# Performance work log

Measured on AMD Instinct MI355X. Metric: run time of the kernel, lower is better.

The kernel has to match this reference:

```python
import jax, jax.numpy as jnp
import numpy as np

TOP_K = 2  # config.num_experts_per_tok


def setup_inputs() -> dict:
    key = jax.random.key(0)
    ks = jax.random.split(key, 5)
    B, S, H, F, E = 1, 2048, 2048, 1408, 8
    sc_h = 1.0 / np.sqrt(H)
    sc_f = 1.0 / np.sqrt(F)
    return {
        "hidden_states": jax.random.normal(ks[0], (B, S, H), jnp.float32),
        "gate_w": jax.random.normal(ks[1], (E, H), jnp.float32) * sc_h,
        "w1": jax.random.normal(ks[2], (E, F, H), jnp.float32) * sc_h,
        "w3": jax.random.normal(ks[3], (E, F, H), jnp.float32) * sc_h,
        "w2": jax.random.normal(ks[4], (E, H, F), jnp.float32) * sc_f,
    }


def reference(hidden_states, gate_w, w1, w3, w2):
    B, S, H = hidden_states.shape
    x = hidden_states.reshape(-1, H)            # [T, H]
    T = x.shape[0]
    E = gate_w.shape[0]

    # Router: logits -> fp32 softmax -> top-k -> renormalize
    router_logits = x @ gate_w.T                # [T, E]
    probs = jax.nn.softmax(router_logits.astype(jnp.float32), axis=-1)
    topk_w, topk_idx = jax.lax.top_k(probs, TOP_K)          # [T, K]
    topk_w = topk_w / topk_w.sum(axis=-1, keepdims=True)
    topk_w = topk_w.astype(x.dtype)

    # Scatter top-k weights into a dense [T, E] combine matrix (zero elsewhere)
    w_full = jnp.zeros((T, E), x.dtype).at[jnp.arange(T)[:, None], topk_idx].add(topk_w)

    # Per-expert SwiGLU MLP applied to all tokens; masked combine honors routing.
    g = jnp.einsum('th,efh->etf', x, w1)        # [E, T, F]
    u = jnp.einsum('th,efh->etf', x, w3)        # [E, T, F]
    h = jax.nn.silu(g) * u                      # [E, T, F]
    y = jnp.einsum('etf,ehf->eth', h, w2)       # [E, T, H]
    out = jnp.einsum('eth,te->th', y, w_full)   # [T, H]

    final_hidden_states = out.reshape(B, S, H)
    return final_hidden_states, router_logits
```

## Files before the change

kernel.cpp:

```cpp
#include <hip/hip_runtime.h>
#include <hip/hip_bf16.h>

#define T_TOK 2048
#define H_DIM 2048
#define F_DIM 1408
#define N_EXP 8
#define BM 128
#define BN 64
#define BK 64

#define NITEM 40
#define G1_NY (F_DIM / BN)
#define G2_NY (H_DIM / BN)
#define G1_CHUNK ((NITEM * G1_NY) / 8)
#define G2_CHUNK ((NITEM * G2_NY) / 8)
#define WELEMS ((size_t)N_EXP * F_DIM * H_DIM)

typedef float f32x4 __attribute__((ext_vector_type(4)));
typedef short s16x8 __attribute__((ext_vector_type(8)));
typedef unsigned int u32;

#define LOFF(row, kbyte) (((row) << 7) + ((kbyte) ^ (((row) & 7) << 4)))

__device__ __forceinline__ int bf2i(__hip_bfloat162 h) {
  int r; __builtin_memcpy(&r, &h, 4); return r;
}

__device__ __forceinline__ int4 pack8(float4 a, float4 b) {
  int4 r;
  r.x = bf2i(__float22bfloat162_rn(float2{a.x, a.y}));
  r.y = bf2i(__float22bfloat162_rn(float2{a.z, a.w}));
  r.z = bf2i(__float22bfloat162_rn(float2{b.x, b.y}));
  r.w = bf2i(__float22bfloat162_rn(float2{b.z, b.w}));
  return r;
}

__device__ __forceinline__ unsigned short f2bf(float f) {
  __hip_bfloat16 h = __float2bfloat16(f);
  unsigned short r; __builtin_memcpy(&r, &h, 2); return r;
}

__device__ __forceinline__ f32x4 mfma16(s16x8 a, s16x8 b, f32x4 c) {
  return __builtin_amdgcn_mfma_f32_16x16x32_bf16(a, b, c, 0, 0, 0);
}

__device__ __forceinline__ void dma16(const unsigned short* g, unsigned short* l) {
  __builtin_amdgcn_global_load_lds((const __attribute__((address_space(1))) u32*)g,
                                   (__attribute__((address_space(3))) u32*)l, 16, 0, 0);
}

__global__ void cast_w3(const float* __restrict__ wa, const float* __restrict__ wb,
                        const float* __restrict__ wc,
                        unsigned short* __restrict__ oa, unsigned short* __restrict__ ob,
                        unsigned short* __restrict__ oc, int n8) {
  const float* in = (blockIdx.y == 0) ? wa : (blockIdx.y == 1) ? wb : wc;
  unsigned short* out = (blockIdx.y == 0) ? oa : (blockIdx.y == 1) ? ob : oc;
  int i = blockIdx.x * blockDim.x + threadIdx.x;
  const int stride = gridDim.x * blockDim.x;
  for (; i < n8; i += stride) {
    const float4 a = ((const float4*)in)[2 * i];
    const float4 b = ((const float4*)in)[2 * i + 1];
    ((int4*)out)[i] = pack8(a, b);
  }
}

__global__ void router_kernel(const float* __restrict__ x, const float* __restrict__ gw,
                              float* __restrict__ logits, int* __restrict__ tk_idx,
                              float* __restrict__ tk_w, unsigned short* __restrict__ xb) {
  __shared__ float xs[H_DIM];
  __shared__ float lg[N_EXP];
  const int t = blockIdx.x;
  const int tid = threadIdx.x;
  const float4 xv = ((const float4*)(x + (size_t)t * H_DIM))[tid];
  ((float4*)xs)[tid] = xv;
  int2 cw;
  cw.x = bf2i(__float22bfloat162_rn(float2{xv.x, xv.y}));
  cw.y = bf2i(__float22bfloat162_rn(float2{xv.z, xv.w}));
  ((int2*)(xb + (size_t)t * H_DIM))[tid] = cw;
  __syncthreads();
  const int w = tid >> 6, l = tid & 63;
  const float* g = gw + w * H_DIM;
  float s = 0.f;
  for (int j = l; j < H_DIM; j += 64) s += xs[j] * g[j];
#pragma unroll
  for (int o = 32; o; o >>= 1) s += __shfl_down(s, o);
  if (l == 0) lg[w] = s;
  __syncthreads();
  if (tid == 0) {
    float mx = lg[0];
#pragma unroll
    for (int i = 1; i < N_EXP; i++) mx = fmaxf(mx, lg[i]);
    float p[N_EXP];
#pragma unroll
    for (int i = 0; i < N_EXP; i++) p[i] = __expf(lg[i] - mx);
    int i0 = 0;
#pragma unroll
    for (int i = 1; i < N_EXP; i++) if (p[i] > p[i0]) i0 = i;
    int i1 = (i0 == 0) ? 1 : 0;
#pragma unroll
    for (int i = 0; i < N_EXP; i++) if (i != i0 && p[i] > p[i1]) i1 = i;
    const float ww = p[i0] + p[i1];
    tk_idx[t * 2] = i0; tk_idx[t * 2 + 1] = i1;
    tk_w[t * 2] = p[i0] / ww; tk_w[t * 2 + 1] = p[i1] / ww;
#pragma unroll
    for (int i = 0; i < N_EXP; i++) logits[t * N_EXP + i] = lg[i];
  }
}

__global__ void build_lists(const int* __restrict__ tk_idx, const float* __restrict__ tk_w,
                            int* __restrict__ counts, int* __restrict__ entries,
                            float* __restrict__ wlist) {
  const int e = blockIdx.x;
  const int l = threadIdx.x;
  int base = 0;
  for (int t0 = 0; t0 < T_TOK; t0 += 64) {
    const int t = t0 + l;
    int sel = -1; float w = 0.f;
    const int i0 = tk_idx[t * 2], i1 = tk_idx[t * 2 + 1];
    if (i0 == e) { sel = t * 2; w = tk_w[t * 2]; }
    else if (i1 == e) { sel = t * 2 + 1; w = tk_w[t * 2 + 1]; }
    const unsigned long long mask = __ballot(sel >= 0);
    const int pos = base + __popcll(mask & ((1ull << l) - 1ull));
    if (sel >= 0) { entries[e * T_TOK + pos] = sel; wlist[e * T_TOK + pos] = w; }
    base += __popcll(mask);
  }
  if (l == 0) counts[e] = base;
}

__global__ void build_items(const int* __restrict__ counts, int* __restrict__ items) {
  if (threadIdx.x == 0) {
    int n = 0;
#pragma unroll
    for (int e = 0; e < N_EXP; e++) {
      const int c = counts[e];
      for (int m0 = 0; m0 < c; m0 += BM) items[1 + n++] = (e << 16) | (m0 / BM);
    }
    items[0] = n;
  }
}

__global__ __launch_bounds__(512)
void moe_gemm1b(const unsigned short* __restrict__ w1b, const unsigned short* __restrict__ w3b,
                const unsigned short* __restrict__ xb,
                const int* __restrict__ counts, const int* __restrict__ entries,
                const int* __restrict__ items,
                unsigned short* __restrict__ hb) {
  const int lin = blockIdx.x;
  const int virt = (lin & 7) * G1_CHUNK + (lin >> 3);
  const int ix = virt % NITEM;
  const int iy = virt / NITEM;
  if (ix >= items[0]) return;
  const int it = items[1 + ix];
  const int e = it >> 16;
  const int m0 = (it & 0xffff) * BM;
  const int rem = counts[e] - m0;
  const int n0 = iy * BN;

  __shared__ unsigned short sA[2][BM * BK];
  __shared__ unsigned short sB1[3][BN * BK];
  __shared__ unsigned short sB3[3][BN * BK];

  const int tid = threadIdx.x;
  const int lane = tid & 63;
  const int wave = tid >> 6;
  const int wm = wave >> 1, wn = wave & 1;

  const int* elist = entries + e * T_TOK + m0;

  const int gcolb = (((lane & 7) << 4) ^ (((lane >> 3) & 7) << 4));
  const int arow0 = wave * 16 + (lane >> 3);
  const int arow1 = arow0 + 8;
  const int tokA0 = elist[arow0 < rem ? arow0 : 0] >> 1;
  const int tokA1 = elist[arow1 < rem ? arow1 : 0] >> 1;
  const unsigned short* gaA0 = xb + (size_t)tokA0 * H_DIM + (gcolb >> 1);
  const unsigned short* gaA1 = xb + (size_t)tokA1 * H_DIM + (gcolb >> 1);
  const int awA = wave * 1024;

  const int rB = tid >> 3;
  const int gbcol = ((tid & 7) ^ (rB & 7)) * 8;
  const unsigned short* gb1 = w1b + ((size_t)e * F_DIM + n0 + rB) * H_DIM + gbcol;
  const unsigned short* gb3 = w3b + ((size_t)e * F_DIM + n0 + rB) * H_DIM + gbcol;
  const int awB = wave * 512;

  const int rowA0 = wm * 32 + (lane & 15);
  const int rowA1 = rowA0 + 16;
  const int rowB0 = wn * 32 + (lane & 15);
  const int rowB1 = rowB0 + 16;
  const int kb = (lane >> 4) * 16;

  const f32x4 zero = {0.f, 0.f, 0.f, 0.f};
  f32x4 aG[2][2], aU[2][2];
#pragma unroll
  for (int i = 0; i < 2; i++)
#pragma unroll
    for (int j = 0; j < 2; j++) { aG[i][j] = zero; aU[i][j] = zero; }

  dma16(gaA0, sA[0] + awA);
  dma16(gaA1, sA[0] + awA + 512);
  dma16(gb1, sB1[0] + awB);
  dma16(gb3, sB3[0] + awB);
  asm volatile("s_waitcnt vmcnt(0)" ::: "memory");
  __builtin_amdgcn_s_barrier();
  dma16(gb1 + BK, sB1[1] + awB);
  dma16(gb3 + BK, sB3[1] + awB);

  const int NT = H_DIM / BK;
  int bi = 0;
  for (int t = 0; t < NT; ++t) {
    const int an = (t + 1) & 1;
    const int bw = (bi + 2 >= 3) ? (bi - 1) : (bi + 2);
    const int ka = (t + 1 < NT) ? (t + 1) * BK : 0;
    const int kbv = (t + 2 < NT) ? (t + 2) * BK : 0;
    dma16(gaA0 + ka, sA[an] + awA);
    dma16(gaA1 + ka, sA[an] + awA + 512);
    dma16(gb1 + kbv, sB1[bw] + awB);
    dma16(gb3 + kbv, sB3[bw] + awB);
    __builtin_amdgcn_sched_barrier(0);
    __builtin_amdgcn_s_setprio(1);
    const char* aC = (const char*)sA[t & 1];
    const char* b1C = (const char*)sB1[bi];
    const char* b3C = (const char*)sB3[bi];
#pragma unroll
    for (int kk = 0; kk < 2; kk++) {
      const int kbyte = kk * 64 + kb;
      const s16x8 a0 = *(const s16x8*)(aC + LOFF(rowA0, kbyte));
      const s16x8 a1 = *(const s16x8*)(aC + LOFF(rowA1, kbyte));
      const s16x8 p0 = *(const s16x8*)(b1C + LOFF(rowB0, kbyte));
      const s16x8 p1 = *(const s16x8*)(b1C + LOFF(rowB1, kbyte));
      const s16x8 q0 = *(const s16x8*)(b3C + LOFF(rowB0, kbyte));
      const s16x8 q1 = *(const s16x8*)(b3C + LOFF(rowB1, kbyte));
      aG[0][0] = mfma16(a0, p0, aG[0][0]); aG[0][1] = mfma16(a0, p1, aG[0][1]);
      aG[1][0] = mfma16(a1, p0, aG[1][0]); aG[1][1] = mfma16(a1, p1, aG[1][1]);
      aU[0][0] = mfma16(a0, q0, aU[0][0]); aU[0][1] = mfma16(a0, q1, aU[0][1]);
      aU[1][0] = mfma16(a1, q0, aU[1][0]); aU[1][1] = mfma16(a1, q1, aU[1][1]);
    }
    __builtin_amdgcn_s_setprio(0);
    asm volatile("s_waitcnt vmcnt(2) lgkmcnt(0)" ::: "memory");
    __builtin_amdgcn_s_barrier();
    bi = (bi + 1 >= 3) ? 0 : (bi + 1);
  }

#pragma unroll
  for (int i = 0; i < 2; i++) {
#pragma unroll
    for (int r = 0; r < 4; r++) {
      const int m = wm * 32 + i * 16 + ((lane >> 4) << 2) + r;
      if (m < rem) {
        const int entry = elist[m];
        unsigned short* hp = hb + (size_t)entry * F_DIM + n0 + wn * 32 + (lane & 15);
#pragma unroll
        for (int j = 0; j < 2; j++) {
          const float g = aG[i][j][r];
          const float u = aU[i][j][r];
          hp[j * 16] = f2bf(g / (1.f + __expf(-g)) * u);
        }
      }
    }
  }
}

__global__ __launch_bounds__(512)
void moe_gemm2b(const unsigned short* __restrict__ w2b,
                const unsigned short* __restrict__ hb,
                const int* __restrict__ counts, const int* __restrict__ entries,
                const float* __restrict__ wlist, const int* __restrict__ items,
                float* __restrict__ out) {
  const int lin = blockIdx.x;
  const int virt = (lin & 7) * G2_CHUNK + (lin >> 3);
  const int ix = virt % NITEM;
  const int iy = virt / NITEM;
  if (ix >= items[0]) return;
  const int it = items[1 + ix];
  const int e = it >> 16;
  const int m0 = (it & 0xffff) * BM;
  const int rem = counts[e] - m0;
  const int n0 = iy * BN;

  __shared__ unsigned short sA[2][BM * BK];
  __shared__ unsigned short sB[3][BN * BK];

  const int tid = threadIdx.x;
  const int lane = tid & 63;
  const int wave = tid >> 6;
  const int wm = wave >> 1, wn = wave & 1;

  const int* elist = entries + e * T_TOK + m0;
  const float* wl = wlist + e * T_TOK + m0;

  const int gcolb = (((lane & 7) << 4) ^ (((lane >> 3) & 7) << 4));
  const int arow0 = wave * 16 + (lane >> 3);
  const int arow1 = arow0 + 8;
  const int enA0 = elist[arow0 < rem ? arow0 : 0];
  const int enA1 = elist[arow1 < rem ? arow1 : 0];
  const unsigned short* gaA0 = hb + (size_t)enA0 * F_DIM + (gcolb >> 1);
  const unsigned short* gaA1 = hb + (size_t)enA1 * F_DIM + (gcolb >> 1);
  const int awA = wave * 1024;

  const int rB = tid >> 3;
  const int gbcol = ((tid & 7) ^ (rB & 7)) * 8;
  const unsigned short* gb = w2b + ((size_t)e * H_DIM + n0 + rB) * F_DIM + gbcol;
  const int awB = wave * 512;

  const int rowA0 = wm * 32 + (lane & 15);
  const int rowA1 = rowA0 + 16;
  const int rowB0 = wn * 32 + (lane & 15);
  const int rowB1 = rowB0 + 16;
  const int kb = (lane >> 4) * 16;

  const f32x4 zero = {0.f, 0.f, 0.f, 0.f};
  f32x4 ac[2][2];
#pragma unroll
  for (int i = 0; i < 2; i++)
#pragma unroll
    for (int j = 0; j < 2; j++) ac[i][j] = zero;

  dma16(gaA0, sA[0] + awA);
  dma16(gaA1, sA[0] + awA + 512);
  dma16(gb, sB[0] + awB);
  asm volatile("s_waitcnt vmcnt(0)" ::: "memory");
  __builtin_amdgcn_s_barrier();
  dma16(gb + BK, sB[1] + awB);

  const int NT = F_DIM / BK;
  int bi = 0;
  for (int t = 0; t < NT; ++t) {
    const int an = (t + 1) & 1;
    const int bw = (bi + 2 >= 3) ? (bi - 1) : (bi + 2);
    const int ka = (t + 1 < NT) ? (t + 1) * BK : 0;
    const int kbv = (t + 2 < NT) ? (t + 2) * BK : 0;
    dma16(gaA0 + ka, sA[an] + awA);
    dma16(gaA1 + ka, sA[an] + awA + 512);
    dma16(gb + kbv, sB[bw] + awB);
    __builtin_amdgcn_sched_barrier(0);
    __builtin_amdgcn_s_setprio(1);
    const char* aC = (const char*)sA[t & 1];
    const char* bC = (const char*)sB[bi];
#pragma unroll
    for (int kk = 0; kk < 2; kk++) {
      const int kbyte = kk * 64 + kb;
      const s16x8 a0 = *(const s16x8*)(aC + LOFF(rowA0, kbyte));
      const s16x8 a1 = *(const s16x8*)(aC + LOFF(rowA1, kbyte));
      const s16x8 f0 = *(const s16x8*)(bC + LOFF(rowB0, kbyte));
      const s16x8 f1 = *(const s16x8*)(bC + LOFF(rowB1, kbyte));
      ac[0][0] = mfma16(a0, f0, ac[0][0]); ac[0][1] = mfma16(a0, f1, ac[0][1]);
      ac[1][0] = mfma16(a1, f0, ac[1][0]); ac[1][1] = mfma16(a1, f1, ac[1][1]);
    }
    __builtin_amdgcn_s_setprio(0);
    asm volatile("s_waitcnt vmcnt(1) lgkmcnt(0)" ::: "memory");
    __builtin_amdgcn_s_barrier();
    bi = (bi + 1 >= 3) ? 0 : (bi + 1);
  }

#pragma unroll
  for (int i = 0; i < 2; i++) {
#pragma unroll
    for (int r = 0; r < 4; r++) {
      const int m = wm * 32 + i * 16 + ((lane >> 4) << 2) + r;
      if (m < rem) {
        const int entry = elist[m];
        const int tok = entry >> 1;
        const float wgt = wl[m];
        float* op = out + (size_t)tok * H_DIM + n0 + wn * 32 + (lane & 15);
#pragma unroll
        for (int j = 0; j < 2; j++) atomicAdd(op + j * 16, wgt * ac[i][j][r]);
      }
    }
  }
}

extern "C" void kernel_launch(void* const* d_in, const int* in_sizes, int n_in,
                              void* d_out, int out_size, void* d_ws, size_t ws_size,
                              hipStream_t stream) {
  const float* x  = (const float*)d_in[0];
  const float* gw = (const float*)d_in[1];
  const float* w1 = (const float*)d_in[2];
  const float* w3 = (const float*)d_in[3];
  const float* w2 = (const float*)d_in[4];
  float* out = (float*)d_out;
  float* logits = out + (size_t)T_TOK * H_DIM;

  char* ws = (char*)d_ws;
  size_t off = 0;
  unsigned short* xb = (unsigned short*)(ws + off); off += (size_t)T_TOK * H_DIM * 2;
  unsigned short* hb = (unsigned short*)(ws + off); off += (size_t)T_TOK * 2 * F_DIM * 2;
  int*   tk_idx = (int*)(ws + off);   off += (size_t)T_TOK * 2 * 4;
  float* tk_w   = (float*)(ws + off); off += (size_t)T_TOK * 2 * 4;
  int*   counts = (int*)(ws + off);   off += 256;
  int*   entries = (int*)(ws + off);  off += (size_t)N_EXP * T_TOK * 4;
  float* wlist  = (float*)(ws + off); off += (size_t)N_EXP * T_TOK * 4;
  int*   items  = (int*)(ws + off);   off += 256;
  unsigned short* w1b = (unsigned short*)(ws + off); off += WELEMS * 2;
  unsigned short* w3b = (unsigned short*)(ws + off); off += WELEMS * 2;
  unsigned short* w2b = (unsigned short*)(ws + off); off += WELEMS * 2;

  (void)hipMemsetAsync(d_out, 0, (size_t)out_size * sizeof(float), stream);
  const int n8 = (int)(WELEMS / 8);
  cast_w3<<<dim3(2048, 3), 256, 0, stream>>>(w1, w3, w2, w1b, w3b, w2b, n8);
  router_kernel<<<dim3(T_TOK), 512, 0, stream>>>(x, gw, logits, tk_idx, tk_w, xb);
  build_lists<<<dim3(N_EXP), 64, 0, stream>>>(tk_idx, tk_w, counts, entries, wlist);
  build_items<<<dim3(1), 64, 0, stream>>>(counts, items);
  moe_gemm1b<<<dim3(NITEM * G1_NY), 512, 0, stream>>>(w1b, w3b, xb, counts, entries, items, hb);
  moe_gemm2b<<<dim3(NITEM * G2_NY), 512, 0, stream>>>(w2b, hb, counts, entries, wlist, items, out);
}
```

Baseline: 285.2 us.

## Fuse w2 fp32-to-bf16 conversion into second GEMM and double-buffer first GEMM

The separate cast pass over w2 is removed. The second expert GEMM now loads fp32 w2 tiles into registers, packs them to bf16 and stores them into LDS, with a register prefetch pipeline spanning two steps. This avoids writing and re-reading a bf16 copy of w2. The first GEMM drops from a triple-buffered to a double-buffered B pipeline that waits on all loads each step, which cuts LDS use but may expose more load latency. The fused path reads w2 in fp32, so each tile fetched by the GEMM carries twice the bytes, and w2 tiles are reread across token blocks.

```diff
diff --git a/kernel.cpp b/kernel.cpp
--- a/kernel.cpp
+++ b/kernel.cpp
@@ -49,12 +49,11 @@
                                    (__attribute__((address_space(3))) u32*)l, 16, 0, 0);
 }
 
-__global__ void cast_w3(const float* __restrict__ wa, const float* __restrict__ wb,
-                        const float* __restrict__ wc,
-                        unsigned short* __restrict__ oa, unsigned short* __restrict__ ob,
-                        unsigned short* __restrict__ oc, int n8) {
-  const float* in = (blockIdx.y == 0) ? wa : (blockIdx.y == 1) ? wb : wc;
-  unsigned short* out = (blockIdx.y == 0) ? oa : (blockIdx.y == 1) ? ob : oc;
+__global__ void cast_w2buf(const float* __restrict__ wa, const float* __restrict__ wb,
+                           unsigned short* __restrict__ oa, unsigned short* __restrict__ ob,
+                           int n8) {
+  const float* in = (blockIdx.y == 0) ? wa : wb;
+  unsigned short* out = (blockIdx.y == 0) ? oa : ob;
   int i = blockIdx.x * blockDim.x + threadIdx.x;
   const int stride = gridDim.x * blockDim.x;
   for (; i < n8; i += stride) {
@@ -157,8 +156,8 @@
   const int n0 = iy * BN;
 
   __shared__ unsigned short sA[2][BM * BK];
-  __shared__ unsigned short sB1[3][BN * BK];
-  __shared__ unsigned short sB3[3][BN * BK];
+  __shared__ unsigned short sB1[2][BN * BK];
+  __shared__ unsigned short sB3[2][BN * BK];
 
   const int tid = threadIdx.x;
   const int lane = tid & 63;
@@ -201,25 +200,20 @@
   dma16(gb3, sB3[0] + awB);
   asm volatile("s_waitcnt vmcnt(0)" ::: "memory");
   __builtin_amdgcn_s_barrier();
-  dma16(gb1 + BK, sB1[1] + awB);
-  dma16(gb3 + BK, sB3[1] + awB);
 
   const int NT = H_DIM / BK;
-  int bi = 0;
   for (int t = 0; t < NT; ++t) {
-    const int an = (t + 1) & 1;
-    const int bw = (bi + 2 >= 3) ? (bi - 1) : (bi + 2);
-    const int ka = (t + 1 < NT) ? (t + 1) * BK : 0;
-    const int kbv = (t + 2 < NT) ? (t + 2) * BK : 0;
-    dma16(gaA0 + ka, sA[an] + awA);
-    dma16(gaA1 + ka, sA[an] + awA + 512);
-    dma16(gb1 + kbv, sB1[bw] + awB);
-    dma16(gb3 + kbv, sB3[bw] + awB);
+    const int cur = t & 1, nxt = cur ^ 1;
+    const int kn = (t + 1 < NT) ? (t + 1) * BK : 0;
+    dma16(gaA0 + kn, sA[nxt] + awA);
+    dma16(gaA1 + kn, sA[nxt] + awA + 512);
+    dma16(gb1 + kn, sB1[nxt] + awB);
+    dma16(gb3 + kn, sB3[nxt] + awB);
     __builtin_amdgcn_sched_barrier(0);
     __builtin_amdgcn_s_setprio(1);
-    const char* aC = (const char*)sA[t & 1];
-    const char* b1C = (const char*)sB1[bi];
-    const char* b3C = (const char*)sB3[bi];
+    const char* aC = (const char*)sA[cur];
+    const char* b1C = (const char*)sB1[cur];
+    const char* b3C = (const char*)sB3[cur];
 #pragma unroll
     for (int kk = 0; kk < 2; kk++) {
       const int kbyte = kk * 64 + kb;
@@ -235,9 +229,8 @@
       aU[1][0] = mfma16(a1, q0, aU[1][0]); aU[1][1] = mfma16(a1, q1, aU[1][1]);
     }
     __builtin_amdgcn_s_setprio(0);
-    asm volatile("s_waitcnt vmcnt(2) lgkmcnt(0)" ::: "memory");
+    asm volatile("s_waitcnt vmcnt(0) lgkmcnt(0)" ::: "memory");
     __builtin_amdgcn_s_barrier();
-    bi = (bi + 1 >= 3) ? 0 : (bi + 1);
   }
 
 #pragma unroll
@@ -259,8 +252,36 @@
   }
 }
 
+#define G2F_STEP(ARD, AWR, BLR, BLW, RS, KA1_, KB3_)                          \
+  {                                                                           \
+    asm volatile("s_waitcnt vmcnt(2) lgkmcnt(0)" ::: "memory");               \
+    __builtin_amdgcn_s_barrier();                                             \
+    *(int4*)((BLW) + offB) = pack8(RS[0], RS[1]);                             \
+    {                                                                         \
+      const int ka = (KA1_);                                                  \
+      dma16(ga0 + ka, (AWR) + aw);                                            \
+      dma16(ga1 + ka, (AWR) + aw + 512);                                      \
+      const int kbl = (KB3_);                                                 \
+      RS[0] = *(const float4*)(pb + kbl);                                     \
+      RS[1] = *(const float4*)(pb + kbl + 4);                                 \
+    }                                                                         \
+    __builtin_amdgcn_sched_barrier(0);                                        \
+    __builtin_amdgcn_s_setprio(1);                                            \
+    _Pragma("unroll")                                                         \
+    for (int kk = 0; kk < 2; kk++) {                                          \
+      const int kbyte = kk * 64 + kb;                                         \
+      const s16x8 a0 = *(const s16x8*)((const char*)(ARD) + LOFF(rowA0, kbyte)); \
+      const s16x8 a1 = *(const s16x8*)((const char*)(ARD) + LOFF(rowA1, kbyte)); \
+      const s16x8 f0 = *(const s16x8*)((BLR) + LOFF(rowB0, kbyte));           \
+      const s16x8 f1 = *(const s16x8*)((BLR) + LOFF(rowB1, kbyte));           \
+      ac[0][0] = mfma16(a0, f0, ac[0][0]); ac[0][1] = mfma16(a0, f1, ac[0][1]); \
+      ac[1][0] = mfma16(a1, f0, ac[1][0]); ac[1][1] = mfma16(a1, f1, ac[1][1]); \
+    }                                                                         \
+    __builtin_amdgcn_s_setprio(0);                                            \
+  }
+
 __global__ __launch_bounds__(512)
-void moe_gemm2b(const unsigned short* __restrict__ w2b,
+void moe_gemm2f(const float* __restrict__ w2,
                 const unsigned short* __restrict__ hb,
                 const int* __restrict__ counts, const int* __restrict__ entries,
                 const float* __restrict__ wlist, const int* __restrict__ items,
@@ -277,7 +298,8 @@
   const int n0 = iy * BN;
 
   __shared__ unsigned short sA[2][BM * BK];
-  __shared__ unsigned short sB[3][BN * BK];
+  __shared__ unsigned short sB[2][BN * BK];
+  char* sb0 = (char*)sB[0]; char* sb1 = (char*)sB[1];
 
   const int tid = threadIdx.x;
   const int lane = tid & 63;
@@ -287,19 +309,19 @@
   const int* elist = entries + e * T_TOK + m0;
   const float* wl = wlist + e * T_TOK + m0;
 
-  const int gcolb = (((lane & 7) << 4) ^ (((lane >> 3) & 7) << 4));
+  const int r0 = tid >> 3;
+  const int gc = tid & 7;
+  const float* pb = w2 + ((size_t)e * H_DIM + n0 + r0) * F_DIM + gc * 8;
+  const int offB = LOFF(r0, gc * 16);
+
   const int arow0 = wave * 16 + (lane >> 3);
   const int arow1 = arow0 + 8;
+  const int gcolb = (((lane & 7) << 4) ^ (((lane >> 3) & 7) << 4));
   const int enA0 = elist[arow0 < rem ? arow0 : 0];
   const int enA1 = elist[arow1 < rem ? arow1 : 0];
-  const unsigned short* gaA0 = hb + (size_t)enA0 * F_DIM + (gcolb >> 1);
-  const unsigned short* gaA1 = hb + (size_t)enA1 * F_DIM + (gcolb >> 1);
-  const int awA = wave * 1024;
-
-  const int rB = tid >> 3;
-  const int gbcol = ((tid & 7) ^ (rB & 7)) * 8;
-  const unsigned short* gb = w2b + ((size_t)e * H_DIM + n0 + rB) * F_DIM + gbcol;
-  const int awB = wave * 512;
+  const unsigned short* ga0 = hb + (size_t)enA0 * F_DIM + (gcolb >> 1);
+  const unsigned short* ga1 = hb + (size_t)enA1 * F_DIM + (gcolb >> 1);
+  const int aw = wave * 1024;
 
   const int rowA0 = wm * 32 + (lane & 15);
   const int rowA1 = rowA0 + 16;
@@ -314,41 +336,23 @@
 #pragma unroll
     for (int j = 0; j < 2; j++) ac[i][j] = zero;
 
-  dma16(gaA0, sA[0] + awA);
-  dma16(gaA1, sA[0] + awA + 512);
-  dma16(gb, sB[0] + awB);
-  asm volatile("s_waitcnt vmcnt(0)" ::: "memory");
-  __builtin_amdgcn_s_barrier();
-  dma16(gb + BK, sB[1] + awB);
+  float4 s1r[2], s0r[2];
+  s1r[0] = *(const float4*)(pb);      s1r[1] = *(const float4*)(pb + 4);
+  s0r[0] = *(const float4*)(pb + BK); s0r[1] = *(const float4*)(pb + BK + 4);
+  dma16(ga0, sA[0] + aw);
+  dma16(ga1, sA[0] + aw + 512);
+  asm volatile("s_waitcnt vmcnt(4)" ::: "memory");
+  *(int4*)(sb0 + offB) = pack8(s1r[0], s1r[1]);
+  s1r[0] = *(const float4*)(pb + 2 * BK); s1r[1] = *(const float4*)(pb + 2 * BK + 4);
 
   const int NT = F_DIM / BK;
-  int bi = 0;
-  for (int t = 0; t < NT; ++t) {
-    const int an = (t + 1) & 1;
-    const int bw = (bi + 2 >= 3) ? (bi - 1) : (bi + 2);
-    const int ka = (t + 1 < NT) ? (t + 1) * BK : 0;
-    const int kbv = (t + 2 < NT) ? (t + 2) * BK : 0;
-    dma16(gaA0 + ka, sA[an] + awA);
-    dma16(gaA1 + ka, sA[an] + awA + 512);
-    dma16(gb + kbv, sB[bw] + awB);
-    __builtin_amdgcn_sched_barrier(0);
-    __builtin_amdgcn_s_setprio(1);
-    const char* aC = (const char*)sA[t & 1];
-    const char* bC = (const char*)sB[bi];
-#pragma unroll
-    for (int kk = 0; kk < 2; kk++) {
-      const int kbyte = kk * 64 + kb;
-      const s16x8 a0 = *(const s16x8*)(aC + LOFF(rowA0, kbyte));
-      const s16x8 a1 = *(const s16x8*)(aC + LOFF(rowA1, kbyte));
-      const s16x8 f0 = *(const s16x8*)(bC + LOFF(rowB0, kbyte));
-      const s16x8 f1 = *(const s16x8*)(bC + LOFF(rowB1, kbyte));
-      ac[0][0] = mfma16(a0, f0, ac[0][0]); ac[0][1] = mfma16(a0, f1, ac[0][1]);
-      ac[1][0] = mfma16(a1, f0, ac[1][0]); ac[1][1] = mfma16(a1, f1, ac[1][1]);
-    }
-    __builtin_amdgcn_s_setprio(0);
-    asm volatile("s_waitcnt vmcnt(1) lgkmcnt(0)" ::: "memory");
-    __builtin_amdgcn_s_barrier();
-    bi = (bi + 1 >= 3) ? 0 : (bi + 1);
+  for (int t = 0; t < NT; t += 2) {
+    const int ka1 = (t + 1 < NT) ? (t + 1) * BK : 0;
+    const int ka2 = (t + 2 < NT) ? (t + 2) * BK : 0;
+    const int kb3 = (t + 3 < NT) ? (t + 3) * BK : 0;
+    const int kb4 = (t + 4 < NT) ? (t + 4) * BK : 0;
+    G2F_STEP(sA[0], sA[1], sb0, sb1, s0r, ka1, kb3);
+    G2F_STEP(sA[1], sA[0], sb1, sb0, s1r, ka2, kb4);
   }
 
 #pragma unroll
@@ -391,14 +395,13 @@
   int*   items  = (int*)(ws + off);   off += 256;
   unsigned short* w1b = (unsigned short*)(ws + off); off += WELEMS * 2;
   unsigned short* w3b = (unsigned short*)(ws + off); off += WELEMS * 2;
-  unsigned short* w2b = (unsigned short*)(ws + off); off += WELEMS * 2;
 
   (void)hipMemsetAsync(d_out, 0, (size_t)out_size * sizeof(float), stream);
   const int n8 = (int)(WELEMS / 8);
-  cast_w3<<<dim3(2048, 3), 256, 0, stream>>>(w1, w3, w2, w1b, w3b, w2b, n8);
+  cast_w2buf<<<dim3(2048, 2), 256, 0, stream>>>(w1, w3, w1b, w3b, n8);
   router_kernel<<<dim3(T_TOK), 512, 0, stream>>>(x, gw, logits, tk_idx, tk_w, xb);
   build_lists<<<dim3(N_EXP), 64, 0, stream>>>(tk_idx, tk_w, counts, entries, wlist);
   build_items<<<dim3(1), 64, 0, stream>>>(counts, items);
   moe_gemm1b<<<dim3(NITEM * G1_NY), 512, 0, stream>>>(w1b, w3b, xb, counts, entries, items, hb);
-  moe_gemm2b<<<dim3(NITEM * G2_NY), 512, 0, stream>>>(w2b, hb, counts, entries, wlist, items, out);
-}
+  moe_gemm2f<<<dim3(NITEM * G2_NY), 512, 0, stream>>>(w2, hb, counts, entries, wlist, items, out);
+}
```

After: 257.7 us. -9.6%, faster.
